# Performance work log

Hardware: AMD Instinct MI355X
Metric: run time of the kernel (lower is better)

The kernel has to match this reference:

```python
import jax, jax.numpy as jnp
import numpy as np

MAX_ATOMS = 50
N_GRAPH_FEAT = 30
N_ATOM_FEAT = 75
BATCH_SIZE = 128
N_ATOMS = MAX_ATOMS * BATCH_SIZE  # 6400 total padded atoms
HIDDEN = 100
N_INPUTS = N_ATOM_FEAT + (MAX_ATOMS - 1) * N_GRAPH_FEAT  # 1545


def setup_inputs() -> dict:
    key = jax.random.key(0)
    ks = jax.random.split(key, 6)
    atom_features = jax.random.normal(ks[0], (N_ATOMS, N_ATOM_FEAT), dtype=jnp.float32)
    parents = jax.random.randint(ks[1], (N_ATOMS, MAX_ATOMS, MAX_ATOMS), 0, MAX_ATOMS + 1, dtype=jnp.int32)
    calculation_orders = jax.random.randint(ks[2], (N_ATOMS, MAX_ATOMS), 0, N_ATOMS, dtype=jnp.int32)
    calculation_masks = jax.random.randint(ks[3], (N_ATOMS, MAX_ATOMS), 0, 2, dtype=jnp.int32) > 0
    # glorot_uniform weights, zero biases (as in build())
    s0 = float(np.sqrt(6.0 / (N_INPUTS + HIDDEN)))
    W0 = jax.random.uniform(ks[4], (N_INPUTS, HIDDEN), jnp.float32, -s0, s0)
    s1 = float(np.sqrt(6.0 / (HIDDEN + N_GRAPH_FEAT)))
    W1 = jax.random.uniform(ks[5], (HIDDEN, N_GRAPH_FEAT), jnp.float32, -s1, s1)
    b0 = jnp.zeros((HIDDEN,), jnp.float32)
    b1 = jnp.zeros((N_GRAPH_FEAT,), jnp.float32)
    return {
        "atom_features": atom_features,
        "parents": parents,
        "calculation_orders": calculation_orders,
        "calculation_masks": calculation_masks,
        "n_atoms": N_ATOMS,
        "W0": W0, "b0": b0, "W1": W1, "b1": b1,
    }


def reference(atom_features, parents, calculation_orders, calculation_masks, n_atoms, W0, b0, W1, b1):
    # Stateful DAG propagation. Original masks out inactive rows per step
    # (dynamic shapes); here we compute all rows and write back the old value
    # for inactive rows, which is the same math under jit.
    rows = jnp.arange(n_atoms)

    def mlp(x):
        h = jax.nn.relu(x @ W0 + b0)
        return jax.nn.relu(h @ W1 + b1)

    gf0 = jnp.zeros((MAX_ATOMS * BATCH_SIZE, MAX_ATOMS + 1, N_GRAPH_FEAT), jnp.float32)
    # per-step slices, leading axis = count
    xs = (parents.transpose(1, 0, 2),       # [T, N, MAX_ATOMS]
          calculation_orders.T,             # [T, N]
          calculation_masks.T)              # [T, N]

    def step(gf, xs_t):
        par, order, mask = xs_t
        batch_atom = atom_features[order]                     # [N, 75]
        # gather parent graph features: gf[row, parent_slot]
        bgf = gf[rows[:, None], par[:, 1:]]                   # [N, 49, 30]
        x = jnp.concatenate([batch_atom, bgf.reshape(n_atoms, -1)], axis=1)  # [N, 1545]
        out = mlp(x)                                          # [N, 30]
        col = par[:, 0]
        old = gf[rows, col]
        new = jnp.where(mask[:, None], out, old)
        gf = gf.at[rows, col].set(new)
        return gf, out

    _, outs = jax.lax.scan(step, gf0, xs)
    out_last = outs[-1]
    # original returns only the masked rows of the last step; zero out inactive
    return jnp.where(calculation_masks[:, -1][:, None], out_last, 0.0)
```

## Files before the change

### kernel.cpp

```cpp
#include <hip/hip_runtime.h>
#include <stdint.h>

#define MA    50
#define NGF   30
#define NAF   75
#define NA    6400
#define H     100
#define RPB   32
#define NTHR  512
#define NT0P  8
#define KT0   52
#define NT1   2
#define KT1   4
#define AFW   104
#define HHW   136

typedef _Float16 f16;
typedef _Float16 f16x8 __attribute__((ext_vector_type(8)));
typedef float    f32x4 __attribute__((ext_vector_type(4)));

#define MFMA16(a, b, c) __builtin_amdgcn_mfma_f32_16x16x32_f16((a), (b), (c), 0, 0, 0)

__global__ void detect_mask(const uint8_t* __restrict__ cm, int* __restrict__ flag) {
    int tid = threadIdx.x;
    int any = 0;
    #pragma unroll
    for (int i = 0; i < 64; ++i) {
        int pos = i * 64 + tid;
        if ((pos & 3) != 0 && cm[pos] != 0) any = 1;
    }
    unsigned long long b = __ballot(any != 0);
    if (tid == 0) *flag = (b != 0ULL) ? 1 : 0;
}

__global__ void pack_w0(const float* __restrict__ W0, f16* __restrict__ ph) {
    int idx = blockIdx.x * 256 + threadIdx.x;
    if (idx >= NT0P * KT0 * 64) return;
    int lane = idx & 63;
    int ktn  = idx >> 6;
    int nt = ktn / KT0, kt = ktn % KT0;
    int col = nt * 16 + (lane & 15);
    #pragma unroll
    for (int e = 0; e < 8; ++e) {
        int k = kt * 32 + (lane >> 4) * 8 + e;
        int kr = -1;
        if (kt < 3) { if (k < NAF) kr = k; }
        else {
            int kk = k - kt * 32;
            if (kk < NGF) kr = NAF + (kt - 3) * NGF + kk;
        }
        float wv = (kr >= 0 && col < H) ? W0[(size_t)kr * H + col] : 0.f;
        ph[(size_t)idx * 8 + e] = (f16)wv;
    }
}

__global__ void pack_w1(const float* __restrict__ W1, f16* __restrict__ ph, f16* __restrict__ pl) {
    int idx = blockIdx.x * 256 + threadIdx.x;
    if (idx >= NT1 * KT1 * 64) return;
    int lane = idx & 63;
    int ktn  = idx >> 6;
    int nt = ktn / KT1, kt = ktn % KT1;
    int col = nt * 16 + (lane & 15);
    #pragma unroll
    for (int e = 0; e < 8; ++e) {
        int k = kt * 32 + (lane >> 4) * 8 + e;
        float wv = (k < H && col < NGF) ? W1[(size_t)k * NGF + col] : 0.f;
        f16 hi = (f16)wv;
        ph[(size_t)idx * 8 + e] = hi;
        pl[(size_t)idx * 8 + e] = (f16)((wv - (float)hi) * 1024.f);
    }
}

__global__ __launch_bounds__(NTHR, 2) void dag_mfma(
    const float* __restrict__ af,
    const int*   __restrict__ parents,
    const int*   __restrict__ orders,
    const void*  __restrict__ cmask,
    const float* __restrict__ b0,
    const float* __restrict__ b1,
    const f16*   __restrict__ w0h,
    const f16*   __restrict__ w1h, const f16* __restrict__ w1l,
    const int*   __restrict__ flagp,
    float*       __restrict__ dout)
{
    __shared__ f16     gfh[51 * 1024];
    __shared__ f16     afh[RPB][AFW];
    __shared__ f16     hh[RPB][HHW];
    __shared__ f32x4   part[4][2][2][64];
    __shared__ float   outl[RPB][33];
    __shared__ uint8_t slots[RPB][52];
    __shared__ int     colc[RPB];
    __shared__ int     maskc[RPB];
    __shared__ int     ordl[2][RPB];

    const int tid   = threadIdx.x;
    const int w     = tid >> 6;
    const int lane  = tid & 63;
    const int mrow  = lane & 15;
    const int kg    = lane >> 4;
    const int npair = w & 3;
    const int half  = w >> 2;
    const int row0  = blockIdx.x * RPB;
    const int flag  = *flagp;

    const int base0 = (mrow * 32 + kg * 8)        ^ ((mrow & 7) << 3);
    const int base1 = ((16 + mrow) * 32 + kg * 8) ^ ((mrow & 7) << 3);

    const int hc0 = npair * 32 + mrow;
    const int hc1 = npair * 32 + 16 + mrow;
    const float b0v0 = (w < 4 && hc0 < H) ? b0[hc0] : 0.f;
    const float b0v1 = (w < 4 && hc1 < H) ? b0[hc1] : 0.f;
    const int oc = (w - 4) * 16 + mrow;
    const float b1v = (w >= 4 && w < 6 && oc < NGF) ? b1[oc] : 0.f;

    {
        f16x8 z = 0;
        for (int e = tid; e < 51 * 128; e += NTHR) ((f16x8*)gfh)[e] = z;
        for (int e = tid; e < RPB * AFW / 8; e += NTHR) ((f16x8*)&afh[0][0])[e] = z;
        for (int e = tid; e < RPB * HHW / 8; e += NTHR) ((f16x8*)&hh[0][0])[e]  = z;
    }
    if (tid >= 384 && tid < 416) {
        int r = tid - 384;
        ordl[0][r] = orders[(size_t)(row0 + r) * MA];
    }
    __syncthreads();

    float afr0 = 0.f, afr1 = 0.f, afr2 = 0.f, afr3 = 0.f, afr4 = 0.f;
    int   slr0 = 0, slr1 = 0, slr2 = 0, slr3 = 0;
    int   colr = 0, mskr = 0, oreg = 0;

    auto LOADS = [&](int T) {
        const int* ordb = ordl[T & 1];
        {
            int idx, r, k;
            idx = tid;        r = idx / NAF; k = idx - r * NAF; afr0 = af[(size_t)ordb[r] * NAF + k];
            idx = tid + 512;  r = idx / NAF; k = idx - r * NAF; afr1 = af[(size_t)ordb[r] * NAF + k];
            idx = tid + 1024; r = idx / NAF; k = idx - r * NAF; afr2 = af[(size_t)ordb[r] * NAF + k];
            idx = tid + 1536; r = idx / NAF; k = idx - r * NAF; afr3 = af[(size_t)ordb[r] * NAF + k];
            if (tid < 352) {
                idx = tid + 2048; r = idx / NAF; k = idx - r * NAF;
                afr4 = af[(size_t)ordb[r] * NAF + k];
            }
        }
        {
            int idx, r, p;
            idx = tid;        r = idx / 49; p = idx - r * 49;
            slr0 = __builtin_nontemporal_load(&parents[((size_t)(row0 + r) * MA + T) * MA + 1 + p]);
            idx = tid + 512;  r = idx / 49; p = idx - r * 49;
            slr1 = __builtin_nontemporal_load(&parents[((size_t)(row0 + r) * MA + T) * MA + 1 + p]);
            idx = tid + 1024; r = idx / 49; p = idx - r * 49;
            slr2 = __builtin_nontemporal_load(&parents[((size_t)(row0 + r) * MA + T) * MA + 1 + p]);
            if (tid < 32) {
                idx = tid + 1536; r = idx / 49; p = idx - r * 49;
                slr3 = __builtin_nontemporal_load(&parents[((size_t)(row0 + r) * MA + T) * MA + 1 + p]);
            }
        }
        if (tid >= 416 && tid < 448) {
            int r = tid - 416;
            colr = __builtin_nontemporal_load(&parents[((size_t)(row0 + r) * MA + T) * MA]);
        }
        if (tid >= 448 && tid < 480) {
            int r = tid - 448;
            if (flag) mskr = (int)__builtin_nontemporal_load(&((const uint8_t*)cmask)[(size_t)(row0 + r) * MA + T]);
            else      mskr = __builtin_nontemporal_load(&((const int*)cmask)[(size_t)(row0 + r) * MA + T]);
        }
        if (T + 1 < MA && tid >= 384 && tid < 416) {
            int r = tid - 384;
            oreg = __builtin_nontemporal_load(&orders[(size_t)(row0 + r) * MA + T + 1]);
        }
    };

    LOADS(0);

    for (int t = 0; t < MA; ++t) {
        {
            int idx, r, k;
            idx = tid;        r = idx / NAF; k = idx - r * NAF; afh[r][k] = (f16)afr0;
            idx = tid + 512;  r = idx / NAF; k = idx - r * NAF; afh[r][k] = (f16)afr1;
            idx = tid + 1024; r = idx / NAF; k = idx - r * NAF; afh[r][k] = (f16)afr2;
            idx = tid + 1536; r = idx / NAF; k = idx - r * NAF; afh[r][k] = (f16)afr3;
            if (tid < 352) { idx = tid + 2048; r = idx / NAF; k = idx - r * NAF; afh[r][k] = (f16)afr4; }
        }
        {
            int idx, r, p;
            idx = tid;        r = idx / 49; p = idx - r * 49; slots[r][p] = (uint8_t)slr0;
            idx = tid + 512;  r = idx / 49; p = idx - r * 49; slots[r][p] = (uint8_t)slr1;
            idx = tid + 1024; r = idx / 49; p = idx - r * 49; slots[r][p] = (uint8_t)slr2;
            if (tid < 32) { idx = tid + 1536; r = idx / 49; p = idx - r * 49; slots[r][p] = (uint8_t)slr3; }
        }
        if (tid >= 416 && tid < 448) colc[tid - 416]  = colr;
        if (tid >= 448 && tid < 480) maskc[tid - 448] = mskr;
        if (t + 1 < MA && tid >= 384 && tid < 416) ordl[(t + 1) & 1][tid - 384] = oreg;
        __syncthreads();

        if (t + 1 < MA) LOADS(t + 1);

        f32x4 acc00 = {0.f,0.f,0.f,0.f}, acc01 = {0.f,0.f,0.f,0.f};
        f32x4 acc10 = {0.f,0.f,0.f,0.f}, acc11 = {0.f,0.f,0.f,0.f};
        {
            const f16x8* B0 = (const f16x8*)w0h + ((size_t)(2 * npair) * KT0 + half * 26) * 64 + lane;
            const f16x8* B1 = B0 + (size_t)KT0 * 64;
            if (half == 0) {
                #pragma unroll
                for (int kt = 0; kt < 3; ++kt) {
                    f16x8 a0 = *(const f16x8*)&afh[mrow][kt * 32 + kg * 8];
                    f16x8 a1 = *(const f16x8*)&afh[16 + mrow][kt * 32 + kg * 8];
                    f16x8 bb0 = B0[(size_t)kt * 64];
                    f16x8 bb1 = B1[(size_t)kt * 64];
                    acc00 = MFMA16(a0, bb0, acc00); acc10 = MFMA16(a1, bb0, acc10);
                    acc01 = MFMA16(a0, bb1, acc01); acc11 = MFMA16(a1, bb1, acc11);
                }
                #pragma unroll
                for (int g = 0; g < 23; ++g) {
                    int s0 = slots[mrow][g];
                    int s1 = slots[16 + mrow][g];
                    f16x8 a0 = *(const f16x8*)&gfh[s0 * 1024 + base0];
                    f16x8 a1 = *(const f16x8*)&gfh[s1 * 1024 + base1];
                    f16x8 bb0 = B0[(size_t)(3 + g) * 64];
                    f16x8 bb1 = B1[(size_t)(3 + g) * 64];
                    acc00 = MFMA16(a0, bb0, acc00); acc10 = MFMA16(a1, bb0, acc10);
                    acc01 = MFMA16(a0, bb1, acc01); acc11 = MFMA16(a1, bb1, acc11);
                }
            } else {
                #pragma unroll
                for (int g = 0; g < 26; ++g) {
                    int s0 = slots[mrow][23 + g];
                    int s1 = slots[16 + mrow][23 + g];
                    f16x8 a0 = *(const f16x8*)&gfh[s0 * 1024 + base0];
                    f16x8 a1 = *(const f16x8*)&gfh[s1 * 1024 + base1];
                    f16x8 bb0 = B0[(size_t)g * 64];
                    f16x8 bb1 = B1[(size_t)g * 64];
                    acc00 = MFMA16(a0, bb0, acc00); acc10 = MFMA16(a1, bb0, acc10);
                    acc01 = MFMA16(a0, bb1, acc01); acc11 = MFMA16(a1, bb1, acc11);
                }
            }
        }
        if (half) {
            part[npair][0][0][lane] = acc00;
            part[npair][0][1][lane] = acc01;
            part[npair][1][0][lane] = acc10;
            part[npair][1][1][lane] = acc11;
        }
        __syncthreads();

        if (!half) {
            acc00 += part[npair][0][0][lane];
            acc01 += part[npair][0][1][lane];
            acc10 += part[npair][1][0][lane];
            acc11 += part[npair][1][1][lane];
            #pragma unroll
            for (int i = 0; i < 4; ++i) {
                hh[kg * 4 + i][hc0]      = (f16)fmaxf(acc00[i] + b0v0, 0.f);
                hh[kg * 4 + i][hc1]      = (f16)fmaxf(acc01[i] + b0v1, 0.f);
                hh[16 + kg * 4 + i][hc0] = (f16)fmaxf(acc10[i] + b0v0, 0.f);
                hh[16 + kg * 4 + i][hc1] = (f16)fmaxf(acc11[i] + b0v1, 0.f);
            }
        }
        __syncthreads();

        if (w == 4 || w == 5) {
            const int nt2 = w - 4;
            f32x4 h00 = {0.f,0.f,0.f,0.f}, l00 = {0.f,0.f,0.f,0.f};
            f32x4 h10 = {0.f,0.f,0.f,0.f}, l10 = {0.f,0.f,0.f,0.f};
            const f16x8* Bh = (const f16x8*)w1h + (size_t)nt2 * KT1 * 64 + lane;
            const f16x8* Bl = (const f16x8*)w1l + (size_t)nt2 * KT1 * 64 + lane;
            #pragma unroll
            for (int kt = 0; kt < KT1; ++kt) {
                f16x8 a0 = *(const f16x8*)&hh[mrow][kt * 32 + kg * 8];
                f16x8 a1 = *(const f16x8*)&hh[16 + mrow][kt * 32 + kg * 8];
                f16x8 bh = Bh[(size_t)kt * 64];
                f16x8 bl = Bl[(size_t)kt * 64];
                h00 = MFMA16(a0, bh, h00); l00 = MFMA16(a0, bl, l00);
                h10 = MFMA16(a1, bh, h10); l10 = MFMA16(a1, bl, l10);
            }
            if (oc < NGF) {
                #pragma unroll
                for (int i = 0; i < 4; ++i) {
                    outl[kg * 4 + i][oc]      = fmaxf(h00[i] + l00[i] * (1.f/1024.f) + b1v, 0.f);
                    outl[16 + kg * 4 + i][oc] = fmaxf(h10[i] + l10[i] * (1.f/1024.f) + b1v, 0.f);
                }
            }
        }
        __syncthreads();

        {
            int e = tid;
            #pragma unroll
            for (int q = 0; q < 2; ++q, e += NTHR) {
                if (e < RPB * NGF) {
                    int r = e / NGF, c = e - r * NGF;
                    float v = outl[r][c];
                    if (maskc[r])
                        gfh[(colc[r] * 1024 + r * 32 + c) ^ ((r & 7) << 3)] = (f16)v;
                    if (t == MA - 1)
                        dout[(size_t)(row0 + r) * NGF + c] = maskc[r] ? v : 0.f;
                }
            }
        }
        __syncthreads();
    }
}

extern "C" void kernel_launch(void* const* d_in, const int* in_sizes, int n_in,
                              void* d_out, int out_size, void* d_ws, size_t ws_size,
                              hipStream_t stream) {
    const float* af      = (const float*)d_in[0];
    const int*   parents = (const int*)  d_in[1];
    const int*   orders  = (const int*)  d_in[2];
    const void*  cmask   =               d_in[3];
    const float* W0      = (const float*)d_in[5];
    const float* b0      = (const float*)d_in[6];
    const float* W1      = (const float*)d_in[7];
    const float* b1      = (const float*)d_in[8];

    char* ws = (char*)d_ws;
    f16* w0h = (f16*)(ws);
    f16* w1h = (f16*)(ws + 425984);
    f16* w1l = (f16*)(ws + 434176);
    int* flagp = (int*)(ws + 442368);
    float* dout = (float*)d_out;

    detect_mask<<<1, 64, 0, stream>>>((const uint8_t*)cmask, flagp);
    pack_w0<<<(NT0P * KT0 * 64 + 255) / 256, 256, 0, stream>>>(W0, w0h);
    pack_w1<<<(NT1 * KT1 * 64 + 255) / 256, 256, 0, stream>>>(W1, w1h, w1l);

    dag_mfma<<<NA / RPB, NTHR, 0, stream>>>(
        af, parents, orders, cmask, b0, b1, w0h, w1h, w1l, flagp, dout);
}
```

Baseline: 289.2 us.

## Repartition layer-0 GEMM to 4-way K split and defer gf scatter

Layer-0 work is reassigned so each wave covers 4 column tiles over a quarter of K instead of 2 column tiles over half of K. The partial sums are then reduced in two stages through shared memory. The scatter of step outputs into the gf state moves into the next iteration's staging phase, which removes one barrier per step, and colc/maskc become double-buffered to support this. Final outputs are written directly from the layer-1 waves. Slot indices are preloaded into registers. The trade is higher register pressure from 8 accumulators and 26 slot registers, plus one extra reduction barrier.

New measurement: 451.0 us. 1.56x slower.

```diff
diff --git a/kernel.cpp b/kernel.cpp
--- a/kernel.cpp
+++ b/kernel.cpp
@@ -86,11 +86,11 @@
     __shared__ f16     gfh[51 * 1024];
     __shared__ f16     afh[RPB][AFW];
     __shared__ f16     hh[RPB][HHW];
-    __shared__ f32x4   part[4][2][2][64];
+    __shared__ f32x4   pbuf[2][2][8][64];
     __shared__ float   outl[RPB][33];
     __shared__ uint8_t slots[RPB][52];
-    __shared__ int     colc[RPB];
-    __shared__ int     maskc[RPB];
+    __shared__ int     colc[2][RPB];
+    __shared__ int     maskc[2][RPB];
     __shared__ int     ordl[2][RPB];
 
     const int tid   = threadIdx.x;
@@ -98,20 +98,22 @@
     const int lane  = tid & 63;
     const int mrow  = lane & 15;
     const int kg    = lane >> 4;
-    const int npair = w & 3;
-    const int half  = w >> 2;
+    const int n     = w >> 2;
+    const int u     = w & 3;
     const int row0  = blockIdx.x * RPB;
     const int flag  = *flagp;
 
-    const int base0 = (mrow * 32 + kg * 8)        ^ ((mrow & 7) << 3);
+    const int base0 = (mrow * 32 + kg * 8) ^ ((mrow & 7) << 3);
     const int base1 = ((16 + mrow) * 32 + kg * 8) ^ ((mrow & 7) << 3);
 
-    const int hc0 = npair * 32 + mrow;
-    const int hc1 = npair * 32 + 16 + mrow;
-    const float b0v0 = (w < 4 && hc0 < H) ? b0[hc0] : 0.f;
-    const float b0v1 = (w < 4 && hc1 < H) ? b0[hc1] : 0.f;
-    const int oc = (w - 4) * 16 + mrow;
-    const float b1v = (w >= 4 && w < 6 && oc < NGF) ? b1[oc] : 0.f;
+    float b0v[4];
+    #pragma unroll
+    for (int j = 0; j < 4; ++j) {
+        int col = n * 64 + j * 16 + mrow;
+        b0v[j] = (u == 0 && col < H) ? b0[col] : 0.f;
+    }
+    const int oc = (w - 2) * 16 + mrow;
+    const float b1v = (w >= 2 && w < 4 && oc < NGF) ? b1[oc] : 0.f;
 
     {
         f16x8 z = 0;
@@ -188,112 +190,152 @@
             idx = tid + 1024; r = idx / 49; p = idx - r * 49; slots[r][p] = (uint8_t)slr2;
             if (tid < 32) { idx = tid + 1536; r = idx / 49; p = idx - r * 49; slots[r][p] = (uint8_t)slr3; }
         }
-        if (tid >= 416 && tid < 448) colc[tid - 416]  = colr;
-        if (tid >= 448 && tid < 480) maskc[tid - 448] = mskr;
+        if (tid >= 416 && tid < 448) colc[t & 1][tid - 416]  = colr;
+        if (tid >= 448 && tid < 480) maskc[t & 1][tid - 448] = mskr;
         if (t + 1 < MA && tid >= 384 && tid < 416) ordl[(t + 1) & 1][tid - 384] = oreg;
+        if (t > 0) {
+            const int tp = (t - 1) & 1;
+            int e = tid;
+            #pragma unroll
+            for (int q = 0; q < 2; ++q, e += NTHR) {
+                if (e < RPB * NGF) {
+                    int r = e / NGF, c = e - r * NGF;
+                    float v = outl[r][c];
+                    if (maskc[tp][r])
+                        gfh[(colc[tp][r] * 1024 + r * 32 + c) ^ ((r & 7) << 3)] = (f16)v;
+                }
+            }
+        }
         __syncthreads();
 
         if (t + 1 < MA) LOADS(t + 1);
 
-        f32x4 acc00 = {0.f,0.f,0.f,0.f}, acc01 = {0.f,0.f,0.f,0.f};
-        f32x4 acc10 = {0.f,0.f,0.f,0.f}, acc11 = {0.f,0.f,0.f,0.f};
-        {
-            const f16x8* B0 = (const f16x8*)w0h + ((size_t)(2 * npair) * KT0 + half * 26) * 64 + lane;
-            const f16x8* B1 = B0 + (size_t)KT0 * 64;
-            if (half == 0) {
+        f32x4 acc[4][2];
+        #pragma unroll
+        for (int j = 0; j < 4; ++j)
+            #pragma unroll
+            for (int m = 0; m < 2; ++m) acc[j][m] = f32x4{0.f, 0.f, 0.f, 0.f};
+
+        int s0r[13], s1r[13];
+        if (u == 0) {
+            #pragma unroll
+            for (int g = 3; g < 13; ++g) { s0r[g] = slots[mrow][g - 3]; s1r[g] = slots[16 + mrow][g - 3]; }
+        } else {
+            const int p0 = u * 13 - 3;
+            #pragma unroll
+            for (int g = 0; g < 13; ++g) { s0r[g] = slots[mrow][p0 + g]; s1r[g] = slots[16 + mrow][p0 + g]; }
+        }
+
+        {
+            const f16x8* Bb = (const f16x8*)w0h + ((size_t)(n * 4) * KT0 + u * 13) * 64 + lane;
+            if (u == 0) {
                 #pragma unroll
                 for (int kt = 0; kt < 3; ++kt) {
                     f16x8 a0 = *(const f16x8*)&afh[mrow][kt * 32 + kg * 8];
                     f16x8 a1 = *(const f16x8*)&afh[16 + mrow][kt * 32 + kg * 8];
-                    f16x8 bb0 = B0[(size_t)kt * 64];
-                    f16x8 bb1 = B1[(size_t)kt * 64];
-                    acc00 = MFMA16(a0, bb0, acc00); acc10 = MFMA16(a1, bb0, acc10);
-                    acc01 = MFMA16(a0, bb1, acc01); acc11 = MFMA16(a1, bb1, acc11);
-                }
-                #pragma unroll
-                for (int g = 0; g < 23; ++g) {
-                    int s0 = slots[mrow][g];
-                    int s1 = slots[16 + mrow][g];
-                    f16x8 a0 = *(const f16x8*)&gfh[s0 * 1024 + base0];
-                    f16x8 a1 = *(const f16x8*)&gfh[s1 * 1024 + base1];
-                    f16x8 bb0 = B0[(size_t)(3 + g) * 64];
-                    f16x8 bb1 = B1[(size_t)(3 + g) * 64];
-                    acc00 = MFMA16(a0, bb0, acc00); acc10 = MFMA16(a1, bb0, acc10);
-                    acc01 = MFMA16(a0, bb1, acc01); acc11 = MFMA16(a1, bb1, acc11);
+                    #pragma unroll
+                    for (int j = 0; j < 4; ++j) {
+                        f16x8 bb = Bb[(size_t)(j * KT0 + kt) * 64];
+                        acc[j][0] = MFMA16(a0, bb, acc[j][0]);
+                        acc[j][1] = MFMA16(a1, bb, acc[j][1]);
+                    }
+                }
+                #pragma unroll
+                for (int g = 3; g < 13; ++g) {
+                    f16x8 a0 = *(const f16x8*)&gfh[s0r[g] * 1024 + base0];
+                    f16x8 a1 = *(const f16x8*)&gfh[s1r[g] * 1024 + base1];
+                    #pragma unroll
+                    for (int j = 0; j < 4; ++j) {
+                        f16x8 bb = Bb[(size_t)(j * KT0 + g) * 64];
+                        acc[j][0] = MFMA16(a0, bb, acc[j][0]);
+                        acc[j][1] = MFMA16(a1, bb, acc[j][1]);
+                    }
                 }
             } else {
                 #pragma unroll
-                for (int g = 0; g < 26; ++g) {
-                    int s0 = slots[mrow][23 + g];
-                    int s1 = slots[16 + mrow][23 + g];
-                    f16x8 a0 = *(const f16x8*)&gfh[s0 * 1024 + base0];
-                    f16x8 a1 = *(const f16x8*)&gfh[s1 * 1024 + base1];
-                    f16x8 bb0 = B0[(size_t)g * 64];
-                    f16x8 bb1 = B1[(size_t)g * 64];
-                    acc00 = MFMA16(a0, bb0, acc00); acc10 = MFMA16(a1, bb0, acc10);
-                    acc01 = MFMA16(a0, bb1, acc01); acc11 = MFMA16(a1, bb1, acc11);
-                }
-            }
-        }
-        if (half) {
-            part[npair][0][0][lane] = acc00;
-            part[npair][0][1][lane] = acc01;
-            part[npair][1][0][lane] = acc10;
-            part[npair][1][1][lane] = acc11;
-        }
-        __syncthreads();
-
-        if (!half) {
-            acc00 += part[npair][0][0][lane];
-            acc01 += part[npair][0][1][lane];
-            acc10 += part[npair][1][0][lane];
-            acc11 += part[npair][1][1][lane];
-            #pragma unroll
-            for (int i = 0; i < 4; ++i) {
-                hh[kg * 4 + i][hc0]      = (f16)fmaxf(acc00[i] + b0v0, 0.f);
-                hh[kg * 4 + i][hc1]      = (f16)fmaxf(acc01[i] + b0v1, 0.f);
-                hh[16 + kg * 4 + i][hc0] = (f16)fmaxf(acc10[i] + b0v0, 0.f);
-                hh[16 + kg * 4 + i][hc1] = (f16)fmaxf(acc11[i] + b0v1, 0.f);
-            }
-        }
-        __syncthreads();
-
-        if (w == 4 || w == 5) {
-            const int nt2 = w - 4;
+                for (int g = 0; g < 13; ++g) {
+                    f16x8 a0 = *(const f16x8*)&gfh[s0r[g] * 1024 + base0];
+                    f16x8 a1 = *(const f16x8*)&gfh[s1r[g] * 1024 + base1];
+                    #pragma unroll
+                    for (int j = 0; j < 4; ++j) {
+                        f16x8 bb = Bb[(size_t)(j * KT0 + g) * 64];
+                        acc[j][0] = MFMA16(a0, bb, acc[j][0]);
+                        acc[j][1] = MFMA16(a1, bb, acc[j][1]);
+                    }
+                }
+            }
+        }
+
+        if (u >= 2) {
+            #pragma unroll
+            for (int j = 0; j < 4; ++j)
+                #pragma unroll
+                for (int m = 0; m < 2; ++m)
+                    pbuf[n][u - 2][j * 2 + m][lane] = acc[j][m];
+        }
+        __syncthreads();
+        if (u < 2) {
+            #pragma unroll
+            for (int j = 0; j < 4; ++j)
+                #pragma unroll
+                for (int m = 0; m < 2; ++m)
+                    acc[j][m] += pbuf[n][u][j * 2 + m][lane];
+            if (u == 1) {
+                #pragma unroll
+                for (int j = 0; j < 4; ++j)
+                    #pragma unroll
+                    for (int m = 0; m < 2; ++m)
+                        pbuf[n][1][j * 2 + m][lane] = acc[j][m];
+            }
+        }
+        __syncthreads();
+        if (u == 0) {
+            #pragma unroll
+            for (int j = 0; j < 4; ++j)
+                #pragma unroll
+                for (int m = 0; m < 2; ++m)
+                    acc[j][m] += pbuf[n][1][j * 2 + m][lane];
+            #pragma unroll
+            for (int j = 0; j < 4; ++j) {
+                int col = n * 64 + j * 16 + mrow;
+                if (col < H) {
+                    #pragma unroll
+                    for (int m = 0; m < 2; ++m)
+                        #pragma unroll
+                        for (int i = 0; i < 4; ++i)
+                            hh[m * 16 + kg * 4 + i][col] = (f16)fmaxf(acc[j][m][i] + b0v[j], 0.f);
+                }
+            }
+        }
+        __syncthreads();
+
+        if (w == 2 || w == 3) {
+            const int nt2 = w - 2;
             f32x4 h00 = {0.f,0.f,0.f,0.f}, l00 = {0.f,0.f,0.f,0.f};
             f32x4 h10 = {0.f,0.f,0.f,0.f}, l10 = {0.f,0.f,0.f,0.f};
             const f16x8* Bh = (const f16x8*)w1h + (size_t)nt2 * KT1 * 64 + lane;
             const f16x8* Bl = (const f16x8*)w1l + (size_t)nt2 * KT1 * 64 + lane;
             #pragma unroll
             for (int kt = 0; kt < KT1; ++kt) {
-                f16x8 a0 = *(const f16x8*)&hh[mrow][kt * 32 + kg * 8];
-                f16x8 a1 = *(const f16x8*)&hh[16 + mrow][kt * 32 + kg * 8];
-                f16x8 bh = Bh[(size_t)kt * 64];
-                f16x8 bl = Bl[(size_t)kt * 64];
-                h00 = MFMA16(a0, bh, h00); l00 = MFMA16(a0, bl, l00);
-                h10 = MFMA16(a1, bh, h10); l10 = MFMA16(a1, bl, l10);
+                f16x8 a0  = *(const f16x8*)&hh[mrow][kt * 32 + kg * 8];
+                f16x8 a1  = *(const f16x8*)&hh[16 + mrow][kt * 32 + kg * 8];
+                f16x8 bhf = Bh[(size_t)kt * 64];
+                f16x8 blf = Bl[(size_t)kt * 64];
+                h00 = MFMA16(a0, bhf, h00); l00 = MFMA16(a0, blf, l00);
+                h10 = MFMA16(a1, bhf, h10); l10 = MFMA16(a1, blf, l10);
             }
             if (oc < NGF) {
                 #pragma unroll
                 for (int i = 0; i < 4; ++i) {
-                    outl[kg * 4 + i][oc]      = fmaxf(h00[i] + l00[i] * (1.f/1024.f) + b1v, 0.f);
-                    outl[16 + kg * 4 + i][oc] = fmaxf(h10[i] + l10[i] * (1.f/1024.f) + b1v, 0.f);
-                }
-            }
-        }
-        __syncthreads();
-
-        {
-            int e = tid;
-            #pragma unroll
-            for (int q = 0; q < 2; ++q, e += NTHR) {
-                if (e < RPB * NGF) {
-                    int r = e / NGF, c = e - r * NGF;
-                    float v = outl[r][c];
-                    if (maskc[r])
-                        gfh[(colc[r] * 1024 + r * 32 + c) ^ ((r & 7) << 3)] = (f16)v;
-                    if (t == MA - 1)
-                        dout[(size_t)(row0 + r) * NGF + c] = maskc[r] ? v : 0.f;
+                    float v0 = fmaxf(h00[i] + l00[i] * (1.f/1024.f) + b1v, 0.f);
+                    float v1 = fmaxf(h10[i] + l10[i] * (1.f/1024.f) + b1v, 0.f);
+                    outl[kg * 4 + i][oc]      = v0;
+                    outl[16 + kg * 4 + i][oc] = v1;
+                    if (t == MA - 1) {
+                        int r0 = kg * 4 + i, r1 = 16 + kg * 4 + i;
+                        dout[(size_t)(row0 + r0) * NGF + oc] = maskc[t & 1][r0] ? v0 : 0.f;
+                        dout[(size_t)(row0 + r1) * NGF + oc] = maskc[t & 1][r1] ? v1 : 0.f;
+                    }
                 }
             }
         }
```

## Fuse prep kernels, defer graph-feature scatter to next step, raise MFMA priority

Applied to the files above, without the earlier changes.

Merges the three small preprocessing kernels (mask detection, W0 and W1 packing) into one launch to cut launch overhead. In the main loop, the scatter of each step's outputs into shared gf is moved into the start of the next iteration, before its existing barrier. This removes one __syncthreads per step, and colc/maskc are double-buffered so the deferred write uses the previous step's values. The final output write moves into the second-layer epilogue, and s_setprio brackets the first-layer MFMA loop to favour those waves.

Measured after the change: 328.9 us. +13.8%, slower.

```diff
diff --git a/kernel.cpp b/kernel.cpp
--- a/kernel.cpp
+++ b/kernel.cpp
@@ -21,53 +21,60 @@
 
 #define MFMA16(a, b, c) __builtin_amdgcn_mfma_f32_16x16x32_f16((a), (b), (c), 0, 0, 0)
 
-__global__ void detect_mask(const uint8_t* __restrict__ cm, int* __restrict__ flag) {
-    int tid = threadIdx.x;
-    int any = 0;
-    #pragma unroll
-    for (int i = 0; i < 64; ++i) {
-        int pos = i * 64 + tid;
-        if ((pos & 3) != 0 && cm[pos] != 0) any = 1;
-    }
-    unsigned long long b = __ballot(any != 0);
-    if (tid == 0) *flag = (b != 0ULL) ? 1 : 0;
-}
-
-__global__ void pack_w0(const float* __restrict__ W0, f16* __restrict__ ph) {
-    int idx = blockIdx.x * 256 + threadIdx.x;
-    if (idx >= NT0P * KT0 * 64) return;
-    int lane = idx & 63;
-    int ktn  = idx >> 6;
-    int nt = ktn / KT0, kt = ktn % KT0;
-    int col = nt * 16 + (lane & 15);
-    #pragma unroll
-    for (int e = 0; e < 8; ++e) {
-        int k = kt * 32 + (lane >> 4) * 8 + e;
-        int kr = -1;
-        if (kt < 3) { if (k < NAF) kr = k; }
-        else {
-            int kk = k - kt * 32;
-            if (kk < NGF) kr = NAF + (kt - 3) * NGF + kk;
-        }
-        float wv = (kr >= 0 && col < H) ? W0[(size_t)kr * H + col] : 0.f;
-        ph[(size_t)idx * 8 + e] = (f16)wv;
-    }
-}
-
-__global__ void pack_w1(const float* __restrict__ W1, f16* __restrict__ ph, f16* __restrict__ pl) {
-    int idx = blockIdx.x * 256 + threadIdx.x;
-    if (idx >= NT1 * KT1 * 64) return;
-    int lane = idx & 63;
-    int ktn  = idx >> 6;
-    int nt = ktn / KT1, kt = ktn % KT1;
-    int col = nt * 16 + (lane & 15);
-    #pragma unroll
-    for (int e = 0; e < 8; ++e) {
-        int k = kt * 32 + (lane >> 4) * 8 + e;
-        float wv = (k < H && col < NGF) ? W1[(size_t)k * NGF + col] : 0.f;
-        f16 hi = (f16)wv;
-        ph[(size_t)idx * 8 + e] = hi;
-        pl[(size_t)idx * 8 + e] = (f16)((wv - (float)hi) * 1024.f);
+__global__ void prep(const float* __restrict__ W0, const float* __restrict__ W1,
+                     const uint8_t* __restrict__ cm,
+                     f16* __restrict__ w0h, f16* __restrict__ w1h, f16* __restrict__ w1l,
+                     int* __restrict__ flag) {
+    const int bid = blockIdx.x;
+    const int tidb = threadIdx.x;
+    if (bid == 0) {
+        if (tidb < 64) {
+            int any = 0;
+            #pragma unroll
+            for (int i = 0; i < 64; ++i) {
+                int pos = i * 64 + tidb;
+                if ((pos & 3) != 0 && cm[pos] != 0) any = 1;
+            }
+            unsigned long long b = __ballot(any != 0);
+            if (tidb == 0) *flag = (b != 0ULL) ? 1 : 0;
+        }
+        return;
+    }
+    if (bid <= 104) {
+        int idx = (bid - 1) * 256 + tidb;
+        int lane = idx & 63;
+        int ktn  = idx >> 6;
+        int nt = ktn / KT0, kt = ktn % KT0;
+        int col = nt * 16 + (lane & 15);
+        #pragma unroll
+        for (int e = 0; e < 8; ++e) {
+            int k = kt * 32 + (lane >> 4) * 8 + e;
+            int kr = -1;
+            if (kt < 3) { if (k < NAF) kr = k; }
+            else {
+                int kk = k - kt * 32;
+                if (kk < NGF) kr = NAF + (kt - 3) * NGF + kk;
+            }
+            float wv = (kr >= 0 && col < H) ? W0[(size_t)kr * H + col] : 0.f;
+            w0h[(size_t)idx * 8 + e] = (f16)wv;
+        }
+        return;
+    }
+    {
+        int idx = (bid - 105) * 256 + tidb;
+        if (idx >= NT1 * KT1 * 64) return;
+        int lane = idx & 63;
+        int ktn  = idx >> 6;
+        int nt = ktn / KT1, kt = ktn % KT1;
+        int col = nt * 16 + (lane & 15);
+        #pragma unroll
+        for (int e = 0; e < 8; ++e) {
+            int k = kt * 32 + (lane >> 4) * 8 + e;
+            float wv = (k < H && col < NGF) ? W1[(size_t)k * NGF + col] : 0.f;
+            f16 hi = (f16)wv;
+            w1h[(size_t)idx * 8 + e] = hi;
+            w1l[(size_t)idx * 8 + e] = (f16)((wv - (float)hi) * 1024.f);
+        }
     }
 }
 
@@ -89,8 +96,8 @@
     __shared__ f32x4   part[4][2][2][64];
     __shared__ float   outl[RPB][33];
     __shared__ uint8_t slots[RPB][52];
-    __shared__ int     colc[RPB];
-    __shared__ int     maskc[RPB];
+    __shared__ int     colc[2][RPB];
+    __shared__ int     maskc[2][RPB];
     __shared__ int     ordl[2][RPB];
 
     const int tid   = threadIdx.x;
@@ -103,7 +110,7 @@
     const int row0  = blockIdx.x * RPB;
     const int flag  = *flagp;
 
-    const int base0 = (mrow * 32 + kg * 8)        ^ ((mrow & 7) << 3);
+    const int base0 = (mrow * 32 + kg * 8) ^ ((mrow & 7) << 3);
     const int base1 = ((16 + mrow) * 32 + kg * 8) ^ ((mrow & 7) << 3);
 
     const int hc0 = npair * 32 + mrow;
@@ -188,15 +195,29 @@
             idx = tid + 1024; r = idx / 49; p = idx - r * 49; slots[r][p] = (uint8_t)slr2;
             if (tid < 32) { idx = tid + 1536; r = idx / 49; p = idx - r * 49; slots[r][p] = (uint8_t)slr3; }
         }
-        if (tid >= 416 && tid < 448) colc[tid - 416]  = colr;
-        if (tid >= 448 && tid < 480) maskc[tid - 448] = mskr;
+        if (tid >= 416 && tid < 448) colc[t & 1][tid - 416]  = colr;
+        if (tid >= 448 && tid < 480) maskc[t & 1][tid - 448] = mskr;
         if (t + 1 < MA && tid >= 384 && tid < 416) ordl[(t + 1) & 1][tid - 384] = oreg;
+        if (t > 0) {
+            const int tp = (t - 1) & 1;
+            int e = tid;
+            #pragma unroll
+            for (int q = 0; q < 2; ++q, e += NTHR) {
+                if (e < RPB * NGF) {
+                    int r = e / NGF, c = e - r * NGF;
+                    float v = outl[r][c];
+                    if (maskc[tp][r])
+                        gfh[(colc[tp][r] * 1024 + r * 32 + c) ^ ((r & 7) << 3)] = (f16)v;
+                }
+            }
+        }
         __syncthreads();
 
         if (t + 1 < MA) LOADS(t + 1);
 
         f32x4 acc00 = {0.f,0.f,0.f,0.f}, acc01 = {0.f,0.f,0.f,0.f};
         f32x4 acc10 = {0.f,0.f,0.f,0.f}, acc11 = {0.f,0.f,0.f,0.f};
+        __builtin_amdgcn_s_setprio(1);
         {
             const f16x8* B0 = (const f16x8*)w0h + ((size_t)(2 * npair) * KT0 + half * 26) * 64 + lane;
             const f16x8* B1 = B0 + (size_t)KT0 * 64;
@@ -235,6 +256,7 @@
                 }
             }
         }
+        __builtin_amdgcn_s_setprio(0);
         if (half) {
             part[npair][0][0][lane] = acc00;
             part[npair][0][1][lane] = acc01;
@@ -266,34 +288,25 @@
             const f16x8* Bl = (const f16x8*)w1l + (size_t)nt2 * KT1 * 64 + lane;
             #pragma unroll
             for (int kt = 0; kt < KT1; ++kt) {
-                f16x8 a0 = *(const f16x8*)&hh[mrow][kt * 32 + kg * 8];
-                f16x8 a1 = *(const f16x8*)&hh[16 + mrow][kt * 32 + kg * 8];
-                f16x8 bh = Bh[(size_t)kt * 64];
-                f16x8 bl = Bl[(size_t)kt * 64];
-                h00 = MFMA16(a0, bh, h00); l00 = MFMA16(a0, bl, l00);
-                h10 = MFMA16(a1, bh, h10); l10 = MFMA16(a1, bl, l10);
+                f16x8 a0  = *(const f16x8*)&hh[mrow][kt * 32 + kg * 8];
+                f16x8 a1  = *(const f16x8*)&hh[16 + mrow][kt * 32 + kg * 8];
+                f16x8 bhf = Bh[(size_t)kt * 64];
+                f16x8 blf = Bl[(size_t)kt * 64];
+                h00 = MFMA16(a0, bhf, h00); l00 = MFMA16(a0, blf, l00);
+                h10 = MFMA16(a1, bhf, h10); l10 = MFMA16(a1, blf, l10);
             }
             if (oc < NGF) {
                 #pragma unroll
                 for (int i = 0; i < 4; ++i) {
-                    outl[kg * 4 + i][oc]      = fmaxf(h00[i] + l00[i] * (1.f/1024.f) + b1v, 0.f);
-                    outl[16 + kg * 4 + i][oc] = fmaxf(h10[i] + l10[i] * (1.f/1024.f) + b1v, 0.f);
-                }
-            }
-        }
-        __syncthreads();
-
-        {
-            int e = tid;
-            #pragma unroll
-            for (int q = 0; q < 2; ++q, e += NTHR) {
-                if (e < RPB * NGF) {
-                    int r = e / NGF, c = e - r * NGF;
-                    float v = outl[r][c];
-                    if (maskc[r])
-                        gfh[(colc[r] * 1024 + r * 32 + c) ^ ((r & 7) << 3)] = (f16)v;
-                    if (t == MA - 1)
-                        dout[(size_t)(row0 + r) * NGF + c] = maskc[r] ? v : 0.f;
+                    float v0 = fmaxf(h00[i] + l00[i] * (1.f/1024.f) + b1v, 0.f);
+                    float v1 = fmaxf(h10[i] + l10[i] * (1.f/1024.f) + b1v, 0.f);
+                    outl[kg * 4 + i][oc]      = v0;
+                    outl[16 + kg * 4 + i][oc] = v1;
+                    if (t == MA - 1) {
+                        int r0 = kg * 4 + i, r1 = 16 + kg * 4 + i;
+                        dout[(size_t)(row0 + r0) * NGF + oc] = maskc[t & 1][r0] ? v0 : 0.f;
+                        dout[(size_t)(row0 + r1) * NGF + oc] = maskc[t & 1][r1] ? v1 : 0.f;
+                    }
                 }
             }
         }
@@ -320,9 +333,7 @@
     int* flagp = (int*)(ws + 442368);
     float* dout = (float*)d_out;
 
-    detect_mask<<<1, 64, 0, stream>>>((const uint8_t*)cmask, flagp);
-    pack_w0<<<(NT0P * KT0 * 64 + 255) / 256, 256, 0, stream>>>(W0, w0h);
-    pack_w1<<<(NT1 * KT1 * 64 + 255) / 256, 256, 0, stream>>>(W1, w1h, w1l);
+    prep<<<107, 256, 0, stream>>>(W0, W1, (const uint8_t*)cmask, w0h, w1h, w1l, flagp);
 
     dag_mfma<<<NA / RPB, NTHR, 0, stream>>>(
         af, parents, orders, cmask, b0, b1, w0h, w1h, w1l, flagp, dout);
```
